# Kernel optimization log

Measured on AMD Instinct MI355X. Metric: run time of the kernel, lower is better.

Reference implementation:

```python
import jax, jax.numpy as jnp
import numpy as np

N_LAYERS = 3
NUM_USERS = 100000
NUM_ITEMS = 50000
N_NODES = NUM_USERS + NUM_ITEMS
N_EDGES = 6000000
EMB = 64


def setup_inputs() -> dict:
    key = jax.random.key(0)
    k1, k2, k3, k4, k5, k6, k7 = jax.random.split(key, 7)
    user_indices = jax.random.randint(k1, (1024,), 0, NUM_USERS)
    item_indices = jax.random.randint(k2, (1024,), 0, NUM_ITEMS)
    adj_src = jax.random.randint(k3, (N_EDGES,), 0, N_NODES)
    adj_dst = jax.random.randint(k4, (N_EDGES,), 0, N_NODES)
    # normalized adjacency values (stand-in for D^-1/2 A D^-1/2 entries)
    adj_vals = jax.random.uniform(k5, (N_EDGES,), dtype=jnp.float32) * 0.05
    user_emb = jax.random.normal(k6, (NUM_USERS, EMB), dtype=jnp.float32) * 0.1
    item_emb = jax.random.normal(k7, (NUM_ITEMS, EMB), dtype=jnp.float32) * 0.1
    return {
        "user_indices": user_indices,
        "item_indices": item_indices,
        "adj_src": adj_src,
        "adj_dst": adj_dst,
        "adj_vals": adj_vals,
        "user_emb": user_emb,
        "item_emb": item_emb,
    }


def reference(user_indices, item_indices, adj_src, adj_dst, adj_vals, user_emb, item_emb):
    # LightGCN.computer(): all_emb = cat(users, items); repeated SpMM; mean over layers
    all_emb = jnp.concatenate([user_emb, item_emb], axis=0)  # [N, d]
    n = all_emb.shape[0]
    cur = all_emb
    acc = all_emb  # running sum over layer embeddings (fused, avoids stacking)
    for _ in range(N_LAYERS):
        # SpMM in COO form: out[dst] += val * cur[src]
        msgs = adj_vals[:, None] * cur[adj_src]  # [E, d]
        cur = jax.ops.segment_sum(msgs, adj_dst, num_segments=n)
        acc = acc + cur
    light_out = acc / jnp.float32(N_LAYERS + 1)  # mean over (n_layers+1) embeddings
    # forward() returns cat(all_users, all_items) == light_out
    return light_out
```

## Files before the change

### kernel.cpp

```cpp
#include <hip/hip_runtime.h>


#define NUM_USERS 100000
#define NUM_ITEMS 50000
#define N_NODES   150000
#define EMB       64
#define N_EDGES   6000000

#define ROWS_PER_B 256
#define NBUCKETS   586
#define NROWS_PAD  (NBUCKETS * ROWS_PER_B)
#define PART_BLOCKS 512
#define CHUNK ((N_EDGES + PART_BLOCKS - 1) / PART_BLOCKS)

constexpr int NODE_F4 = N_NODES * EMB / 4;
constexpr int USER_F4 = NUM_USERS * EMB / 4;

__device__ __forceinline__ float bf2f(unsigned short u) {
    union { unsigned int i; float f; } x; x.i = ((unsigned int)u) << 16; return x.f;
}
__device__ __forceinline__ unsigned short f2bf(float f) {
    union { float f; unsigned int i; } x; x.f = f;
    unsigned int b = x.i;
    return (unsigned short)((b + 0x7FFFu + ((b >> 16) & 1u)) >> 16);
}


__global__ void k_zero(int* __restrict__ p, int n) {
    int i = blockIdx.x * blockDim.x + threadIdx.x;
    if (i < n) p[i] = 0;
}

__global__ __launch_bounds__(256) void k_bhist(const int* __restrict__ dst,
                                               int* __restrict__ gcnt) {
    __shared__ int cnt[NBUCKETS];
    int t = threadIdx.x;
    for (int i = t; i < NBUCKETS; i += 256) cnt[i] = 0;
    __syncthreads();
    int e0 = blockIdx.x * CHUNK;
    int e1 = min(e0 + CHUNK, N_EDGES);
    int e = e0 + t;
    for (; e + 256 < e1; e += 512) {
        int b0 = dst[e] >> 8;
        int b1 = dst[e + 256] >> 8;
        atomicAdd(&cnt[b0], 1);
        atomicAdd(&cnt[b1], 1);
    }
    if (e < e1) atomicAdd(&cnt[dst[e] >> 8], 1);
    __syncthreads();
    for (int i = t; i < NBUCKETS; i += 256)
        if (cnt[i]) atomicAdd(&gcnt[i], cnt[i]);
}

__global__ void k_bscan(const int* __restrict__ gcnt, int* __restrict__ boff,
                        int* __restrict__ gcur) {
    __shared__ int s[1024];
    int t = threadIdx.x;
    int x = (t < NBUCKETS) ? gcnt[t] : 0;
    s[t] = x;
    __syncthreads();
    for (int off = 1; off < 1024; off <<= 1) {
        int v = (t >= off) ? s[t - off] : 0;
        __syncthreads();
        s[t] += v;
        __syncthreads();
    }
    if (t < NBUCKETS) { int ex = s[t] - x; boff[t] = ex; gcur[t] = ex; }
    if (t == 0) boff[NBUCKETS] = N_EDGES;
}


__global__ __launch_bounds__(256) void k_part(const int* __restrict__ src,
                                              const int* __restrict__ dst,
                                              const float* __restrict__ val,
                                              int* __restrict__ gcur,
                                              int2* __restrict__ pairs) {
    __shared__ int cnt[NBUCKETS];
    __shared__ int base[NBUCKETS];
    int t = threadIdx.x;
    for (int i = t; i < NBUCKETS; i += 256) cnt[i] = 0;
    __syncthreads();
    int e0 = blockIdx.x * CHUNK;
    int e1 = min(e0 + CHUNK, N_EDGES);
    {
        int e = e0 + t;
        for (; e + 256 < e1; e += 512) {
            int b0 = dst[e] >> 8;
            int b1 = dst[e + 256] >> 8;
            atomicAdd(&cnt[b0], 1);
            atomicAdd(&cnt[b1], 1);
        }
        if (e < e1) atomicAdd(&cnt[dst[e] >> 8], 1);
    }
    __syncthreads();
    for (int i = t; i < NBUCKETS; i += 256) {
        int c = cnt[i];
        base[i] = c ? atomicAdd(&gcur[i], c) : 0;
        cnt[i] = 0;
    }
    __syncthreads();
    {
        int e = e0 + t;
        for (; e + 256 < e1; e += 512) {
            int d0 = dst[e];       int s0 = src[e];       float v0 = val[e];
            int d1 = dst[e + 256]; int s1 = src[e + 256]; float v1 = val[e + 256];
            int b0 = d0 >> 8, b1 = d1 >> 8;
            int o0 = atomicAdd(&cnt[b0], 1);
            int o1 = atomicAdd(&cnt[b1], 1);
            pairs[base[b0] + o0] = make_int2(s0 | ((d0 & 255) << 18), __float_as_int(v0));
            pairs[base[b1] + o1] = make_int2(s1 | ((d1 & 255) << 18), __float_as_int(v1));
        }
        if (e < e1) {
            int d0 = dst[e];
            int o0 = atomicAdd(&cnt[d0 >> 8], 1);
            pairs[base[d0 >> 8] + o0] = make_int2(src[e] | ((d0 & 255) << 18),
                                                  __float_as_int(val[e]));
        }
    }
}


__global__ __launch_bounds__(256) void k_sort(const int* __restrict__ boff,
                                              const int2* __restrict__ pairs1,
                                              int2* __restrict__ pairs2,
                                              int* __restrict__ row_ptr) {
    __shared__ int cnt[ROWS_PER_B];
    __shared__ int s[ROWS_PER_B];
    int b = blockIdx.x;
    int t = threadIdx.x;
    cnt[t] = 0;
    __syncthreads();
    int beg = boff[b], end = boff[b + 1];
    {
        int e = beg + t;
        for (; e + 256 < end; e += 512) {
            int r0 = ((unsigned)pairs1[e].x) >> 18;
            int r1 = ((unsigned)pairs1[e + 256].x) >> 18;
            atomicAdd(&cnt[r0], 1);
            atomicAdd(&cnt[r1], 1);
        }
        if (e < end) atomicAdd(&cnt[((unsigned)pairs1[e].x) >> 18], 1);
    }
    __syncthreads();
    int x = cnt[t];
    s[t] = x;
    __syncthreads();
    for (int off = 1; off < 256; off <<= 1) {
        int v = (t >= off) ? s[t - off] : 0;
        __syncthreads();
        s[t] += v;
        __syncthreads();
    }
    int ex = beg + s[t] - x;
    row_ptr[b * ROWS_PER_B + t] = ex;
    if (b == NBUCKETS - 1 && t == 255) row_ptr[NROWS_PAD] = N_EDGES;
    __syncthreads();
    cnt[t] = ex;
    __syncthreads();
    {
        int e = beg + t;
        for (; e + 256 < end; e += 512) {
            int2 p0 = pairs1[e];
            int2 p1 = pairs1[e + 256];
            int pos0 = atomicAdd(&cnt[((unsigned)p0.x) >> 18], 1);
            int pos1 = atomicAdd(&cnt[((unsigned)p1.x) >> 18], 1);
            pairs2[pos0] = make_int2(p0.x & 0x3FFFF, p0.y);
            pairs2[pos1] = make_int2(p1.x & 0x3FFFF, p1.y);
        }
        if (e < end) {
            int2 p0 = pairs1[e];
            int pos0 = atomicAdd(&cnt[((unsigned)p0.x) >> 18], 1);
            pairs2[pos0] = make_int2(p0.x & 0x3FFFF, p0.y);
        }
    }
}


__global__ void k_init(const float4* __restrict__ ue, const float4* __restrict__ ie,
                       ushort4* __restrict__ curb, float4* __restrict__ acc) {
    int i = blockIdx.x * blockDim.x + threadIdx.x;
    if (i >= NODE_F4) return;
    float4 v = (i < USER_F4) ? ue[i] : ie[i - USER_F4];
    acc[i] = v;
    curb[i] = make_ushort4(f2bf(v.x), f2bf(v.y), f2bf(v.z), f2bf(v.w));
}

__global__ __launch_bounds__(256) void k_spmm(const int* __restrict__ row_ptr,
                                              const int2* __restrict__ pairs,
                                              const ushort4* __restrict__ cur,
                                              ushort4* __restrict__ nxt,
                                              float4* __restrict__ acc, float s) {
    int tid = blockIdx.x * blockDim.x + threadIdx.x;
    int row = tid >> 4;
    if (row >= N_NODES) return;
    int c = tid & 15;
    int beg = row_ptr[row];
    int end = row_ptr[row + 1];
    float4 r = make_float4(0.f, 0.f, 0.f, 0.f);
    int k = beg;
    for (; k + 3 < end; k += 4) {
        int2 p0 = pairs[k];
        int2 p1 = pairs[k + 1];
        int2 p2 = pairs[k + 2];
        int2 p3 = pairs[k + 3];
        ushort4 g0 = cur[(long)p0.x * 16 + c];
        ushort4 g1 = cur[(long)p1.x * 16 + c];
        ushort4 g2 = cur[(long)p2.x * 16 + c];
        ushort4 g3 = cur[(long)p3.x * 16 + c];
        float v0 = __int_as_float(p0.y);
        float v1 = __int_as_float(p1.y);
        float v2 = __int_as_float(p2.y);
        float v3 = __int_as_float(p3.y);
        r.x += v0 * bf2f(g0.x) + v1 * bf2f(g1.x) + v2 * bf2f(g2.x) + v3 * bf2f(g3.x);
        r.y += v0 * bf2f(g0.y) + v1 * bf2f(g1.y) + v2 * bf2f(g2.y) + v3 * bf2f(g3.y);
        r.z += v0 * bf2f(g0.z) + v1 * bf2f(g1.z) + v2 * bf2f(g2.z) + v3 * bf2f(g3.z);
        r.w += v0 * bf2f(g0.w) + v1 * bf2f(g1.w) + v2 * bf2f(g2.w) + v3 * bf2f(g3.w);
    }
    for (; k < end; ++k) {
        int2 p0 = pairs[k];
        ushort4 g0 = cur[(long)p0.x * 16 + c];
        float v0 = __int_as_float(p0.y);
        r.x += v0 * bf2f(g0.x);
        r.y += v0 * bf2f(g0.y);
        r.z += v0 * bf2f(g0.z);
        r.w += v0 * bf2f(g0.w);
    }
    long o = (long)row * 16 + c;
    nxt[o] = make_ushort4(f2bf(r.x), f2bf(r.y), f2bf(r.z), f2bf(r.w));
    float4 a = acc[o];
    a.x = (a.x + r.x) * s;
    a.y = (a.y + r.y) * s;
    a.z = (a.z + r.z) * s;
    a.w = (a.w + r.w) * s;
    acc[o] = a;
}


__global__ void lgcn_init(const float4* __restrict__ user_emb,
                          const float4* __restrict__ item_emb,
                          float4* __restrict__ cur, float4* __restrict__ nxt,
                          float4* __restrict__ acc) {
    int i = blockIdx.x * blockDim.x + threadIdx.x;
    if (i >= NODE_F4) return;
    float4 v = (i < USER_F4) ? user_emb[i] : item_emb[i - USER_F4];
    cur[i] = v; acc[i] = v; nxt[i] = make_float4(0.f, 0.f, 0.f, 0.f);
}

__global__ void lgcn_scatter(const int* __restrict__ src, const int* __restrict__ dst,
                             const float* __restrict__ val,
                             const float4* __restrict__ cur, float* __restrict__ nxt) {
    int tid = blockIdx.x * blockDim.x + threadIdx.x;
    int e = tid >> 4;
    if (e >= N_EDGES) return;
    int c = tid & 15;
    int s = src[e]; int d = dst[e]; float v = val[e];
    float4 m = cur[(long)s * 16 + c];
    float* p = nxt + (long)d * 64 + c * 4;
    unsafeAtomicAdd(p + 0, v * m.x);
    unsafeAtomicAdd(p + 1, v * m.y);
    unsafeAtomicAdd(p + 2, v * m.z);
    unsafeAtomicAdd(p + 3, v * m.w);
}

__global__ void lgcn_add_zero(float4* __restrict__ acc, const float4* __restrict__ nxt,
                              float4* __restrict__ other) {
    int i = blockIdx.x * blockDim.x + threadIdx.x;
    if (i >= NODE_F4) return;
    float4 a = acc[i]; float4 n = nxt[i];
    a.x += n.x; a.y += n.y; a.z += n.z; a.w += n.w;
    acc[i] = a;
    other[i] = make_float4(0.f, 0.f, 0.f, 0.f);
}

__global__ void lgcn_final(float4* __restrict__ acc, const float4* __restrict__ nxt) {
    int i = blockIdx.x * blockDim.x + threadIdx.x;
    if (i >= NODE_F4) return;
    float4 a = acc[i]; float4 n = nxt[i];
    a.x = (a.x + n.x) * 0.25f; a.y = (a.y + n.y) * 0.25f;
    a.z = (a.z + n.z) * 0.25f; a.w = (a.w + n.w) * 0.25f;
    acc[i] = a;
}


extern "C" void kernel_launch(void* const* d_in, const int* in_sizes, int n_in,
                              void* d_out, int out_size, void* d_ws, size_t ws_size,
                              hipStream_t stream) {
    const int*    adj_src  = (const int*)d_in[2];
    const int*    adj_dst  = (const int*)d_in[3];
    const float*  adj_vals = (const float*)d_in[4];
    const float4* user_emb = (const float4*)d_in[5];
    const float4* item_emb = (const float4*)d_in[6];
    float* acc = (float*)d_out;

    const int BLK = 256;
    const int grid_node  = (NODE_F4 + BLK - 1) / BLK;
    const int grid_row16 = (N_NODES * 16 + BLK - 1) / BLK;

    const size_t SZ_PAIRS = (size_t)N_EDGES * 8;
    const size_t SZ_BF    = (size_t)N_NODES * EMB * 2;
    const size_t SZ_RP    = 600320;
    const size_t SZ_B     = 4096;
    const size_t NEEDED   = 2 * SZ_PAIRS + SZ_RP + 3 * SZ_B;

    if (ws_size >= NEEDED) {
        char* w = (char*)d_ws;
        int2*    pairs2  = (int2*)(w);
        int2*    pairs1  = (int2*)(w + SZ_PAIRS);
        ushort4* curb    = (ushort4*)(w + SZ_PAIRS);
        ushort4* nxtb    = (ushort4*)(w + SZ_PAIRS + SZ_BF);
        int*     row_ptr = (int*)(w + 2 * SZ_PAIRS);
        int*     gcnt    = (int*)(w + 2 * SZ_PAIRS + SZ_RP);
        int*     boff    = (int*)(w + 2 * SZ_PAIRS + SZ_RP + SZ_B);
        int*     gcur    = (int*)(w + 2 * SZ_PAIRS + SZ_RP + 2 * SZ_B);

        k_zero<<<(NBUCKETS + BLK - 1) / BLK, BLK, 0, stream>>>(gcnt, NBUCKETS);
        k_bhist<<<PART_BLOCKS, BLK, 0, stream>>>(adj_dst, gcnt);
        k_bscan<<<1, 1024, 0, stream>>>(gcnt, boff, gcur);

        k_part<<<PART_BLOCKS, BLK, 0, stream>>>(adj_src, adj_dst, adj_vals, gcur, pairs1);

        k_sort<<<NBUCKETS, BLK, 0, stream>>>(boff, pairs1, pairs2, row_ptr);

        k_init<<<grid_node, BLK, 0, stream>>>(user_emb, item_emb, curb, (float4*)acc);
        k_spmm<<<grid_row16, BLK, 0, stream>>>(row_ptr, pairs2, curb, nxtb,
                                               (float4*)acc, 1.0f);
        k_spmm<<<grid_row16, BLK, 0, stream>>>(row_ptr, pairs2, nxtb, curb,
                                               (float4*)acc, 1.0f);
        k_spmm<<<grid_row16, BLK, 0, stream>>>(row_ptr, pairs2, curb, nxtb,
                                               (float4*)acc, 0.25f);
    } else {
        float* ws0 = (float*)d_ws;
        float* ws1 = ws0 + (size_t)N_NODES * EMB;
        lgcn_init<<<grid_node, BLK, 0, stream>>>(user_emb, item_emb,
                                                 (float4*)ws0, (float4*)ws1, (float4*)acc);
        lgcn_scatter<<<(N_EDGES*16+BLK-1)/BLK, BLK, 0, stream>>>(adj_src, adj_dst, adj_vals,
                                                    (const float4*)ws0, ws1);
        lgcn_add_zero<<<grid_node, BLK, 0, stream>>>((float4*)acc, (const float4*)ws1, (float4*)ws0);
        lgcn_scatter<<<(N_EDGES*16+BLK-1)/BLK, BLK, 0, stream>>>(adj_src, adj_dst, adj_vals,
                                                    (const float4*)ws1, ws0);
        lgcn_add_zero<<<grid_node, BLK, 0, stream>>>((float4*)acc, (const float4*)ws0, (float4*)ws1);
        lgcn_scatter<<<(N_EDGES*16+BLK-1)/BLK, BLK, 0, stream>>>(adj_src, adj_dst, adj_vals,
                                                    (const float4*)ws0, ws1);
        lgcn_final<<<grid_node, BLK, 0, stream>>>((float4*)acc, (const float4*)ws1);
    }
}
```

Baseline: 681.2 us.

## Widen SpMM gathers to 16B, defer accumulator updates, add nontemporal loads

The SpMM now uses 8 threads per row, each gathering 8 bf16 values (16 bytes) per edge instead of 4. The first two layers no longer read and write the fp32 accumulator; they only write bf16 layer outputs into separate buffers. A final fused kernel sums the accumulator with the saved layer-1 and layer-2 bf16 embeddings and applies the mean. Streaming loads in the partition, sort and SpMM kernels are marked nontemporal to keep gather data in cache. The cost is an extra bf16 buffer in the workspace, and layer outputs now enter the mean at bf16 rather than fp32 precision.

```diff
diff --git a/kernel.cpp b/kernel.cpp
--- a/kernel.cpp
+++ b/kernel.cpp
@@ -16,6 +16,9 @@
 constexpr int NODE_F4 = N_NODES * EMB / 4;
 constexpr int USER_F4 = NUM_USERS * EMB / 4;
 
+typedef unsigned short us8 __attribute__((ext_vector_type(8)));
+typedef float f4v __attribute__((ext_vector_type(4)));
+
 __device__ __forceinline__ float bf2f(unsigned short u) {
     union { unsigned int i; float f; } x; x.i = ((unsigned int)u) << 16; return x.f;
 }
@@ -41,12 +44,12 @@
     int e1 = min(e0 + CHUNK, N_EDGES);
     int e = e0 + t;
     for (; e + 256 < e1; e += 512) {
-        int b0 = dst[e] >> 8;
-        int b1 = dst[e + 256] >> 8;
+        int b0 = __builtin_nontemporal_load(dst + e) >> 8;
+        int b1 = __builtin_nontemporal_load(dst + e + 256) >> 8;
         atomicAdd(&cnt[b0], 1);
         atomicAdd(&cnt[b1], 1);
     }
-    if (e < e1) atomicAdd(&cnt[dst[e] >> 8], 1);
+    if (e < e1) atomicAdd(&cnt[__builtin_nontemporal_load(dst + e) >> 8], 1);
     __syncthreads();
     for (int i = t; i < NBUCKETS; i += 256)
         if (cnt[i]) atomicAdd(&gcnt[i], cnt[i]);
@@ -85,12 +88,12 @@
     {
         int e = e0 + t;
         for (; e + 256 < e1; e += 512) {
-            int b0 = dst[e] >> 8;
-            int b1 = dst[e + 256] >> 8;
+            int b0 = __builtin_nontemporal_load(dst + e) >> 8;
+            int b1 = __builtin_nontemporal_load(dst + e + 256) >> 8;
             atomicAdd(&cnt[b0], 1);
             atomicAdd(&cnt[b1], 1);
         }
-        if (e < e1) atomicAdd(&cnt[dst[e] >> 8], 1);
+        if (e < e1) atomicAdd(&cnt[__builtin_nontemporal_load(dst + e) >> 8], 1);
     }
     __syncthreads();
     for (int i = t; i < NBUCKETS; i += 256) {
@@ -102,8 +105,12 @@
     {
         int e = e0 + t;
         for (; e + 256 < e1; e += 512) {
-            int d0 = dst[e];       int s0 = src[e];       float v0 = val[e];
-            int d1 = dst[e + 256]; int s1 = src[e + 256]; float v1 = val[e + 256];
+            int d0 = __builtin_nontemporal_load(dst + e);
+            int s0 = __builtin_nontemporal_load(src + e);
+            float v0 = __builtin_nontemporal_load(val + e);
+            int d1 = __builtin_nontemporal_load(dst + e + 256);
+            int s1 = __builtin_nontemporal_load(src + e + 256);
+            float v1 = __builtin_nontemporal_load(val + e + 256);
             int b0 = d0 >> 8, b1 = d1 >> 8;
             int o0 = atomicAdd(&cnt[b0], 1);
             int o1 = atomicAdd(&cnt[b1], 1);
@@ -111,10 +118,12 @@
             pairs[base[b1] + o1] = make_int2(s1 | ((d1 & 255) << 18), __float_as_int(v1));
         }
         if (e < e1) {
-            int d0 = dst[e];
+            int d0 = __builtin_nontemporal_load(dst + e);
+            int s0 = __builtin_nontemporal_load(src + e);
+            float v0 = __builtin_nontemporal_load(val + e);
             int o0 = atomicAdd(&cnt[d0 >> 8], 1);
-            pairs[base[d0 >> 8] + o0] = make_int2(src[e] | ((d0 & 255) << 18),
-                                                  __float_as_int(val[e]));
+            pairs[base[d0 >> 8] + o0] = make_int2(s0 | ((d0 & 255) << 18),
+                                                  __float_as_int(v0));
         }
     }
 }
@@ -157,82 +166,140 @@
     __syncthreads();
     cnt[t] = ex;
     __syncthreads();
+    const long* p1l = (const long*)pairs1;
     {
         int e = beg + t;
         for (; e + 256 < end; e += 512) {
-            int2 p0 = pairs1[e];
-            int2 p1 = pairs1[e + 256];
-            int pos0 = atomicAdd(&cnt[((unsigned)p0.x) >> 18], 1);
-            int pos1 = atomicAdd(&cnt[((unsigned)p1.x) >> 18], 1);
-            pairs2[pos0] = make_int2(p0.x & 0x3FFFF, p0.y);
-            pairs2[pos1] = make_int2(p1.x & 0x3FFFF, p1.y);
+            long q0 = __builtin_nontemporal_load(p1l + e);
+            long q1 = __builtin_nontemporal_load(p1l + e + 256);
+            int x0 = (int)q0, y0 = (int)(q0 >> 32);
+            int x1 = (int)q1, y1 = (int)(q1 >> 32);
+            int pos0 = atomicAdd(&cnt[((unsigned)x0) >> 18], 1);
+            int pos1 = atomicAdd(&cnt[((unsigned)x1) >> 18], 1);
+            pairs2[pos0] = make_int2(x0 & 0x3FFFF, y0);
+            pairs2[pos1] = make_int2(x1 & 0x3FFFF, y1);
         }
         if (e < end) {
-            int2 p0 = pairs1[e];
-            int pos0 = atomicAdd(&cnt[((unsigned)p0.x) >> 18], 1);
-            pairs2[pos0] = make_int2(p0.x & 0x3FFFF, p0.y);
-        }
-    }
-}
-
-
-__global__ void k_init(const float4* __restrict__ ue, const float4* __restrict__ ie,
-                       ushort4* __restrict__ curb, float4* __restrict__ acc) {
+            long q0 = __builtin_nontemporal_load(p1l + e);
+            int x0 = (int)q0, y0 = (int)(q0 >> 32);
+            int pos0 = atomicAdd(&cnt[((unsigned)x0) >> 18], 1);
+            pairs2[pos0] = make_int2(x0 & 0x3FFFF, y0);
+        }
+    }
+}
+
+
+__global__ void k_init(const f4v* __restrict__ ue, const f4v* __restrict__ ie,
+                       ushort4* __restrict__ e0b, f4v* __restrict__ acc) {
     int i = blockIdx.x * blockDim.x + threadIdx.x;
     if (i >= NODE_F4) return;
-    float4 v = (i < USER_F4) ? ue[i] : ie[i - USER_F4];
-    acc[i] = v;
-    curb[i] = make_ushort4(f2bf(v.x), f2bf(v.y), f2bf(v.z), f2bf(v.w));
+    f4v v = (i < USER_F4) ? __builtin_nontemporal_load(ue + i)
+                          : __builtin_nontemporal_load(ie + i - USER_F4);
+    __builtin_nontemporal_store(v, acc + i);
+    e0b[i] = make_ushort4(f2bf(v.x), f2bf(v.y), f2bf(v.z), f2bf(v.w));
 }
 
 __global__ __launch_bounds__(256) void k_spmm(const int* __restrict__ row_ptr,
-                                              const int2* __restrict__ pairs,
-                                              const ushort4* __restrict__ cur,
-                                              ushort4* __restrict__ nxt,
-                                              float4* __restrict__ acc, float s) {
+                                              const long* __restrict__ pairs,
+                                              const us8* __restrict__ cur,
+                                              us8* __restrict__ nxt) {
     int tid = blockIdx.x * blockDim.x + threadIdx.x;
-    int row = tid >> 4;
+    int row = tid >> 3;
     if (row >= N_NODES) return;
-    int c = tid & 15;
+    int c = tid & 7;
     int beg = row_ptr[row];
     int end = row_ptr[row + 1];
-    float4 r = make_float4(0.f, 0.f, 0.f, 0.f);
+    float r[8];
+#pragma unroll
+    for (int j = 0; j < 8; ++j) r[j] = 0.f;
     int k = beg;
     for (; k + 3 < end; k += 4) {
-        int2 p0 = pairs[k];
-        int2 p1 = pairs[k + 1];
-        int2 p2 = pairs[k + 2];
-        int2 p3 = pairs[k + 3];
-        ushort4 g0 = cur[(long)p0.x * 16 + c];
-        ushort4 g1 = cur[(long)p1.x * 16 + c];
-        ushort4 g2 = cur[(long)p2.x * 16 + c];
-        ushort4 g3 = cur[(long)p3.x * 16 + c];
-        float v0 = __int_as_float(p0.y);
-        float v1 = __int_as_float(p1.y);
-        float v2 = __int_as_float(p2.y);
-        float v3 = __int_as_float(p3.y);
-        r.x += v0 * bf2f(g0.x) + v1 * bf2f(g1.x) + v2 * bf2f(g2.x) + v3 * bf2f(g3.x);
-        r.y += v0 * bf2f(g0.y) + v1 * bf2f(g1.y) + v2 * bf2f(g2.y) + v3 * bf2f(g3.y);
-        r.z += v0 * bf2f(g0.z) + v1 * bf2f(g1.z) + v2 * bf2f(g2.z) + v3 * bf2f(g3.z);
-        r.w += v0 * bf2f(g0.w) + v1 * bf2f(g1.w) + v2 * bf2f(g2.w) + v3 * bf2f(g3.w);
+        long p0 = __builtin_nontemporal_load(pairs + k);
+        long p1 = __builtin_nontemporal_load(pairs + k + 1);
+        long p2 = __builtin_nontemporal_load(pairs + k + 2);
+        long p3 = __builtin_nontemporal_load(pairs + k + 3);
+        us8 g0 = cur[(long)(int)(p0 & 0x3FFFF) * 8 + c];
+        us8 g1 = cur[(long)(int)(p1 & 0x3FFFF) * 8 + c];
+        us8 g2 = cur[(long)(int)(p2 & 0x3FFFF) * 8 + c];
+        us8 g3 = cur[(long)(int)(p3 & 0x3FFFF) * 8 + c];
+        float v0 = __int_as_float((int)(p0 >> 32));
+        float v1 = __int_as_float((int)(p1 >> 32));
+        float v2 = __int_as_float((int)(p2 >> 32));
+        float v3 = __int_as_float((int)(p3 >> 32));
+#pragma unroll
+        for (int j = 0; j < 8; ++j)
+            r[j] += v0 * bf2f(g0[j]) + v1 * bf2f(g1[j])
+                  + v2 * bf2f(g2[j]) + v3 * bf2f(g3[j]);
     }
     for (; k < end; ++k) {
-        int2 p0 = pairs[k];
-        ushort4 g0 = cur[(long)p0.x * 16 + c];
-        float v0 = __int_as_float(p0.y);
-        r.x += v0 * bf2f(g0.x);
-        r.y += v0 * bf2f(g0.y);
-        r.z += v0 * bf2f(g0.z);
-        r.w += v0 * bf2f(g0.w);
-    }
-    long o = (long)row * 16 + c;
-    nxt[o] = make_ushort4(f2bf(r.x), f2bf(r.y), f2bf(r.z), f2bf(r.w));
-    float4 a = acc[o];
-    a.x = (a.x + r.x) * s;
-    a.y = (a.y + r.y) * s;
-    a.z = (a.z + r.z) * s;
-    a.w = (a.w + r.w) * s;
-    acc[o] = a;
+        long p0 = __builtin_nontemporal_load(pairs + k);
+        us8 g0 = cur[(long)(int)(p0 & 0x3FFFF) * 8 + c];
+        float v0 = __int_as_float((int)(p0 >> 32));
+#pragma unroll
+        for (int j = 0; j < 8; ++j) r[j] += v0 * bf2f(g0[j]);
+    }
+    us8 o;
+#pragma unroll
+    for (int j = 0; j < 8; ++j) o[j] = f2bf(r[j]);
+    nxt[(long)row * 8 + c] = o;
+}
+
+__global__ __launch_bounds__(256) void k_spmm_fin(const int* __restrict__ row_ptr,
+                                                  const long* __restrict__ pairs,
+                                                  const us8* __restrict__ cur,
+                                                  const us8* __restrict__ e1b,
+                                                  float4* __restrict__ acc) {
+    int tid = blockIdx.x * blockDim.x + threadIdx.x;
+    int row = tid >> 3;
+    if (row >= N_NODES) return;
+    int c = tid & 7;
+    int beg = row_ptr[row];
+    int end = row_ptr[row + 1];
+    float r[8];
+#pragma unroll
+    for (int j = 0; j < 8; ++j) r[j] = 0.f;
+    int k = beg;
+    for (; k + 3 < end; k += 4) {
+        long p0 = __builtin_nontemporal_load(pairs + k);
+        long p1 = __builtin_nontemporal_load(pairs + k + 1);
+        long p2 = __builtin_nontemporal_load(pairs + k + 2);
+        long p3 = __builtin_nontemporal_load(pairs + k + 3);
+        us8 g0 = cur[(long)(int)(p0 & 0x3FFFF) * 8 + c];
+        us8 g1 = cur[(long)(int)(p1 & 0x3FFFF) * 8 + c];
+        us8 g2 = cur[(long)(int)(p2 & 0x3FFFF) * 8 + c];
+        us8 g3 = cur[(long)(int)(p3 & 0x3FFFF) * 8 + c];
+        float v0 = __int_as_float((int)(p0 >> 32));
+        float v1 = __int_as_float((int)(p1 >> 32));
+        float v2 = __int_as_float((int)(p2 >> 32));
+        float v3 = __int_as_float((int)(p3 >> 32));
+#pragma unroll
+        for (int j = 0; j < 8; ++j)
+            r[j] += v0 * bf2f(g0[j]) + v1 * bf2f(g1[j])
+                  + v2 * bf2f(g2[j]) + v3 * bf2f(g3[j]);
+    }
+    for (; k < end; ++k) {
+        long p0 = __builtin_nontemporal_load(pairs + k);
+        us8 g0 = cur[(long)(int)(p0 & 0x3FFFF) * 8 + c];
+        float v0 = __int_as_float((int)(p0 >> 32));
+#pragma unroll
+        for (int j = 0; j < 8; ++j) r[j] += v0 * bf2f(g0[j]);
+    }
+    long o8 = (long)row * 8 + c;
+    us8 e1 = e1b[o8];
+    us8 e2 = cur[o8];
+    long oa = (long)row * 16 + c * 2;
+    float4 a0 = acc[oa];
+    float4 a1 = acc[oa + 1];
+    a0.x = (a0.x + bf2f(e1[0]) + bf2f(e2[0]) + r[0]) * 0.25f;
+    a0.y = (a0.y + bf2f(e1[1]) + bf2f(e2[1]) + r[1]) * 0.25f;
+    a0.z = (a0.z + bf2f(e1[2]) + bf2f(e2[2]) + r[2]) * 0.25f;
+    a0.w = (a0.w + bf2f(e1[3]) + bf2f(e2[3]) + r[3]) * 0.25f;
+    a1.x = (a1.x + bf2f(e1[4]) + bf2f(e2[4]) + r[4]) * 0.25f;
+    a1.y = (a1.y + bf2f(e1[5]) + bf2f(e2[5]) + r[5]) * 0.25f;
+    a1.z = (a1.z + bf2f(e1[6]) + bf2f(e2[6]) + r[6]) * 0.25f;
+    a1.w = (a1.w + bf2f(e1[7]) + bf2f(e2[7]) + r[7]) * 0.25f;
+    acc[oa] = a0;
+    acc[oa + 1] = a1;
 }
 
 
@@ -288,30 +355,29 @@
     const int*    adj_src  = (const int*)d_in[2];
     const int*    adj_dst  = (const int*)d_in[3];
     const float*  adj_vals = (const float*)d_in[4];
-    const float4* user_emb = (const float4*)d_in[5];
-    const float4* item_emb = (const float4*)d_in[6];
     float* acc = (float*)d_out;
 
     const int BLK = 256;
-    const int grid_node  = (NODE_F4 + BLK - 1) / BLK;
-    const int grid_row16 = (N_NODES * 16 + BLK - 1) / BLK;
+    const int grid_node = (NODE_F4 + BLK - 1) / BLK;
+    const int grid_row8 = (N_NODES * 8 + BLK - 1) / BLK;
 
     const size_t SZ_PAIRS = (size_t)N_EDGES * 8;
     const size_t SZ_BF    = (size_t)N_NODES * EMB * 2;
     const size_t SZ_RP    = 600320;
     const size_t SZ_B     = 4096;
-    const size_t NEEDED   = 2 * SZ_PAIRS + SZ_RP + 3 * SZ_B;
+    const size_t NEEDED   = 2 * SZ_PAIRS + SZ_BF + SZ_RP + 3 * SZ_B;
 
     if (ws_size >= NEEDED) {
         char* w = (char*)d_ws;
-        int2*    pairs2  = (int2*)(w);
-        int2*    pairs1  = (int2*)(w + SZ_PAIRS);
-        ushort4* curb    = (ushort4*)(w + SZ_PAIRS);
-        ushort4* nxtb    = (ushort4*)(w + SZ_PAIRS + SZ_BF);
-        int*     row_ptr = (int*)(w + 2 * SZ_PAIRS);
-        int*     gcnt    = (int*)(w + 2 * SZ_PAIRS + SZ_RP);
-        int*     boff    = (int*)(w + 2 * SZ_PAIRS + SZ_RP + SZ_B);
-        int*     gcur    = (int*)(w + 2 * SZ_PAIRS + SZ_RP + 2 * SZ_B);
+        int2* pairs2 = (int2*)(w);
+        int2* pairs1 = (int2*)(w + SZ_PAIRS);
+        us8*  e0b    = (us8*)(w + SZ_PAIRS);
+        us8*  e1b    = (us8*)(w + SZ_PAIRS + SZ_BF);
+        us8*  e2b    = (us8*)(w + 2 * SZ_PAIRS);
+        int*  row_ptr= (int*)(w + 2 * SZ_PAIRS + SZ_BF);
+        int*  gcnt   = (int*)(w + 2 * SZ_PAIRS + SZ_BF + SZ_RP);
+        int*  boff   = (int*)(w + 2 * SZ_PAIRS + SZ_BF + SZ_RP + SZ_B);
+        int*  gcur   = (int*)(w + 2 * SZ_PAIRS + SZ_BF + SZ_RP + 2 * SZ_B);
 
         k_zero<<<(NBUCKETS + BLK - 1) / BLK, BLK, 0, stream>>>(gcnt, NBUCKETS);
         k_bhist<<<PART_BLOCKS, BLK, 0, stream>>>(adj_dst, gcnt);
@@ -321,14 +387,15 @@
 
         k_sort<<<NBUCKETS, BLK, 0, stream>>>(boff, pairs1, pairs2, row_ptr);
 
-        k_init<<<grid_node, BLK, 0, stream>>>(user_emb, item_emb, curb, (float4*)acc);
-        k_spmm<<<grid_row16, BLK, 0, stream>>>(row_ptr, pairs2, curb, nxtb,
-                                               (float4*)acc, 1.0f);
-        k_spmm<<<grid_row16, BLK, 0, stream>>>(row_ptr, pairs2, nxtb, curb,
-                                               (float4*)acc, 1.0f);
-        k_spmm<<<grid_row16, BLK, 0, stream>>>(row_ptr, pairs2, curb, nxtb,
-                                               (float4*)acc, 0.25f);
+        k_init<<<grid_node, BLK, 0, stream>>>((const f4v*)d_in[5], (const f4v*)d_in[6],
+                                              (ushort4*)e0b, (f4v*)acc);
+        k_spmm<<<grid_row8, BLK, 0, stream>>>(row_ptr, (const long*)pairs2, e0b, e1b);
+        k_spmm<<<grid_row8, BLK, 0, stream>>>(row_ptr, (const long*)pairs2, e1b, e2b);
+        k_spmm_fin<<<grid_row8, BLK, 0, stream>>>(row_ptr, (const long*)pairs2, e2b,
+                                                  e1b, (float4*)acc);
     } else {
+        const float4* user_emb = (const float4*)d_in[5];
+        const float4* item_emb = (const float4*)d_in[6];
         float* ws0 = (float*)d_ws;
         float* ws1 = ws0 + (size_t)N_NODES * EMB;
         lgcn_init<<<grid_node, BLK, 0, stream>>>(user_emb, item_emb,
```

Result: slower. 786.5 us (+15.5%).
